# Optimization experiments

Hardware: AMD Instinct MI355X
Metric: run time of the kernel (lower is better)

Reference implementation:

```python
import jax, jax.numpy as jnp
import numpy as np

NEG_INF = -1e30  # mask value used by QANet's apply_mask


def setup_inputs() -> dict:
    key = jax.random.key(0)
    ks = jax.random.split(key, 6)
    B, C, Q, H = 64, 1024, 128, 512
    return {
        "x_context": jax.random.normal(ks[0], (B, C, H), dtype=jnp.float32),
        "x_query": jax.random.normal(ks[1], (B, Q, H), dtype=jnp.float32),
        "context_mask": jnp.ones((B, C), dtype=jnp.float32),
        "query_mask": jnp.ones((B, Q), dtype=jnp.float32),
        "W0": jax.random.normal(ks[2], (H,), dtype=jnp.float32) * 0.05,
        "W1": jax.random.normal(ks[3], (H,), dtype=jnp.float32) * 0.05,
        "W2": jax.random.normal(ks[4], (H,), dtype=jnp.float32) * 0.05,
        "bias": jnp.zeros((1,), dtype=jnp.float32),
    }


def reference(x_context, x_query, context_mask, query_mask, W0, W1, W2, bias):
    # Trilinear similarity S[b,c,q] = q.W0 + c.W1 + (q*W2).c + bias
    # (original computes [B,Q,C] then transposes; we build [B,C,Q] directly)
    sub0 = jnp.einsum('bqh,h->bq', x_query, W0)          # [B,Q]
    sub1 = jnp.einsum('bch,h->bc', x_context, W1)        # [B,C]
    sub2 = jnp.einsum('bch,bqh->bcq', x_context, x_query * W2)  # [B,C,Q]
    S = sub2 + sub1[:, :, None] + sub0[:, None, :] + bias  # [B,C,Q]

    mq = query_mask[:, None, :]    # [B,1,Q]
    mc = context_mask[:, :, None]  # [B,C,1]

    # context-to-query: softmax over query axis, masked by query_mask
    S_ = jax.nn.softmax(S + (1.0 - mq) * NEG_INF, axis=-1)  # [B,C,Q]
    c2q = jnp.einsum('bcq,bqh->bch', S_, x_query)           # [B,C,H]

    # query-to-context: softmax over context axis, masked by context_mask
    S_c = jax.nn.softmax(S + (1.0 - mc) * NEG_INF, axis=1)  # [B,C,Q]
    S_T = jnp.swapaxes(S_c, 1, 2)                            # [B,Q,C]
    # (S_ @ S_T) @ x_context, associated as S_ @ (S_T @ x_context)
    tmp = jnp.einsum('bqc,bch->bqh', S_T, x_context)        # [B,Q,H]
    q2c = jnp.einsum('bcq,bqh->bch', S_, tmp)               # [B,C,H]
    return c2q, q2c
```

## Files before the change

### kernel.cpp

```cpp
#include <hip/hip_runtime.h>

#define BB 64
#define CC 1024
#define QQ 128
#define HH 512

typedef short bf16x8 __attribute__((ext_vector_type(8)));
typedef float f32x4 __attribute__((ext_vector_type(4)));

#define GLD16(g, l)                                                            \
    __builtin_amdgcn_global_load_lds(                                          \
        (const __attribute__((address_space(1))) unsigned int*)(g),            \
        (__attribute__((address_space(3))) unsigned int*)(l), 16, 0, 0)

__device__ __forceinline__ unsigned short f2bf(float f) {
    unsigned u = __float_as_uint(f);
    u += 0x7FFF + ((u >> 16) & 1);
    return (unsigned short)(u >> 16);
}
__device__ __forceinline__ unsigned pk2(float lo, float hi) {
    return (unsigned)f2bf(lo) | ((unsigned)f2bf(hi) << 16);
}

__global__ __launch_bounds__(256) void k_sub0(const float* __restrict__ xq,
                                              const float* __restrict__ w0,
                                              float* __restrict__ sub0,
                                              float* __restrict__ colsum) {
    if (blockIdx.x < 32) colsum[blockIdx.x * 256 + threadIdx.x] = 0.0f;
    int wave = threadIdx.x >> 6;
    int lane = threadIdx.x & 63;
    int row  = blockIdx.x * 4 + wave;
    const float* p = xq + (size_t)row * HH + lane * 8;
    float4 a0 = *(const float4*)(p);
    float4 a1 = *(const float4*)(p + 4);
    float4 b0 = *(const float4*)(w0 + lane * 8);
    float4 b1 = *(const float4*)(w0 + lane * 8 + 4);
    float s = a0.x*b0.x + a0.y*b0.y + a0.z*b0.z + a0.w*b0.w
            + a1.x*b1.x + a1.y*b1.y + a1.z*b1.z + a1.w*b1.w;
    #pragma unroll
    for (int off = 32; off; off >>= 1) s += __shfl_xor(s, off);
    if (lane == 0) sub0[row] = s;
}

__global__ __launch_bounds__(256) void k_prep(const float* __restrict__ xq,
                                              const float* __restrict__ w2,
                                              const float* __restrict__ qmask,
                                              unsigned short* __restrict__ xqw2b,
                                              unsigned short* __restrict__ xqmT) {
    int b  = blockIdx.y;
    int ht = blockIdx.x * 128;
    int tid = threadIdx.x;
    __shared__ __align__(16) unsigned short sT[128][132];

    {
        int q  = tid >> 1;
        int hh = (tid & 1) * 64;
        float qm = qmask[b * QQ + q];
        const float* xp = xq + ((size_t)b * QQ + q) * HH + ht + hh;
        unsigned short* wr = xqw2b + ((size_t)b * QQ + q) * HH + ht + hh;
        #pragma unroll
        for (int i = 0; i < 16; i++) {
            float4 v = *(const float4*)(xp + i * 4);
            float4 w = *(const float4*)(w2 + ht + hh + i * 4);
            uint2 pw; pw.x = pk2(v.x * w.x, v.y * w.y);
                      pw.y = pk2(v.z * w.z, v.w * w.w);
            *(uint2*)(wr + i * 4) = pw;
            uint2 pm; pm.x = pk2(v.x * qm, v.y * qm);
                      pm.y = pk2(v.z * qm, v.w * qm);
            *(uint2*)(&sT[q][hh + i * 4]) = pm;
        }
    }
    __syncthreads();
    {
        int h  = tid >> 1;
        int qh = (tid & 1) * 64;
        unsigned short* orow = xqmT + ((size_t)b * HH + ht + h) * QQ + qh;
        #pragma unroll
        for (int i = 0; i < 8; i++) {
            uint4 o;
            o.x = (unsigned)sT[qh + i*8 + 0][h] | ((unsigned)sT[qh + i*8 + 1][h] << 16);
            o.y = (unsigned)sT[qh + i*8 + 2][h] | ((unsigned)sT[qh + i*8 + 3][h] << 16);
            o.z = (unsigned)sT[qh + i*8 + 4][h] | ((unsigned)sT[qh + i*8 + 5][h] << 16);
            o.w = (unsigned)sT[qh + i*8 + 6][h] | ((unsigned)sT[qh + i*8 + 7][h] << 16);
            *(uint4*)(orow + i * 8) = o;
        }
    }
}

__global__ __launch_bounds__(256) void k_scores(
    const float* __restrict__ xc, const unsigned short* __restrict__ xqw2b,
    const float* __restrict__ w1, const float* __restrict__ cmask,
    const float* __restrict__ qmask, const float* __restrict__ bias,
    const float* __restrict__ sub0, unsigned short* __restrict__ Ebf,
    float* __restrict__ rowsum, float* __restrict__ colsum) {
    int b  = blockIdx.y;
    int c0 = blockIdx.x * 128;
    int tid  = threadIdx.x;
    int lane = tid & 63, wave = tid >> 6;
    int quad = lane >> 4, lcol = lane & 15;
    int wrow = (wave >> 1) * 64, wcol = (wave & 1) * 64;

    __shared__ __align__(16) unsigned short sA[128][32];
    __shared__ __align__(16) unsigned short sB[128][32];
    __shared__ float sW1[512];
    __shared__ float sSub1[128];
    __shared__ float sS0[128], sQm[128], sCm[128];
    __shared__ float sRowP[2][128], sColP[2][128];

    sW1[tid] = w1[tid]; sW1[tid + 256] = w1[tid + 256];
    if (tid < 128) {
        sS0[tid] = sub0[b * QQ + tid] + bias[0];
        sQm[tid] = qmask[b * QQ + tid];
        sCm[tid] = cmask[b * CC + c0 + tid];
    }

    f32x4 acc[4][4];
    #pragma unroll
    for (int i = 0; i < 4; i++)
        #pragma unroll
        for (int j = 0; j < 4; j++) acc[i][j] = (f32x4)0.0f;
    float s1 = 0.0f;

    int arow = tid >> 1, akh = (tid & 1) * 16;

    for (int k0 = 0; k0 < HH; k0 += 32) {
        __syncthreads();
        {
            const float* gp = xc + ((size_t)(b * CC + c0 + arow)) * HH + k0 + akh;
            float4 v0 = *(const float4*)(gp);
            float4 v1 = *(const float4*)(gp + 4);
            float4 v2 = *(const float4*)(gp + 8);
            float4 v3 = *(const float4*)(gp + 12);
            const float* wp = sW1 + k0 + akh;
            s1 += v0.x*wp[0] + v0.y*wp[1] + v0.z*wp[2] + v0.w*wp[3]
                + v1.x*wp[4] + v1.y*wp[5] + v1.z*wp[6] + v1.w*wp[7]
                + v2.x*wp[8] + v2.y*wp[9] + v2.z*wp[10] + v2.w*wp[11]
                + v3.x*wp[12] + v3.y*wp[13] + v3.z*wp[14] + v3.w*wp[15];
            uint4 p0, p1;
            p0.x = pk2(v0.x, v0.y); p0.y = pk2(v0.z, v0.w);
            p0.z = pk2(v1.x, v1.y); p0.w = pk2(v1.z, v1.w);
            p1.x = pk2(v2.x, v2.y); p1.y = pk2(v2.z, v2.w);
            p1.z = pk2(v3.x, v3.y); p1.w = pk2(v3.z, v3.w);
            *(uint4*)&sA[arow][akh]     = p0;
            *(uint4*)&sA[arow][akh + 8] = p1;
        }
        #pragma unroll
        for (int j = 0; j < 2; j++) {
            int chunk = wave * 2 + j;
            int row = chunk * 16 + (lane >> 2);
            GLD16(xqw2b + ((size_t)b * QQ + row) * HH + k0 + (lane & 3) * 8,
                  (unsigned short*)sB + chunk * 512);
        }
        __syncthreads();
        bf16x8 af[4];
        #pragma unroll
        for (int mi = 0; mi < 4; mi++)
            af[mi] = *(const bf16x8*)&sA[wrow + mi * 16 + lcol][quad * 8];
        #pragma unroll
        for (int ni = 0; ni < 4; ni++) {
            bf16x8 bfr = *(const bf16x8*)&sB[wcol + ni * 16 + lcol][quad * 8];
            #pragma unroll
            for (int mi = 0; mi < 4; mi++)
                acc[mi][ni] = __builtin_amdgcn_mfma_f32_16x16x32_bf16(
                    af[mi], bfr, acc[mi][ni], 0, 0, 0);
        }
    }

    s1 += __shfl_xor(s1, 1);
    if ((tid & 1) == 0) sSub1[arow] = s1;
    __syncthreads();

    float rsp[4][4];
    float csp[4] = {0.f, 0.f, 0.f, 0.f};
    #pragma unroll
    for (int mi = 0; mi < 4; mi++)
        #pragma unroll
        for (int r = 0; r < 4; r++) rsp[mi][r] = 0.f;

    #pragma unroll
    for (int mi = 0; mi < 4; mi++) {
        #pragma unroll
        for (int ni = 0; ni < 4; ni++) {
            int col = wcol + ni * 16 + lcol;
            float qm = sQm[col], s0 = sS0[col];
            #pragma unroll
            for (int r = 0; r < 4; r++) {
                int row = wrow + mi * 16 + quad * 4 + r;
                float e = __expf(acc[mi][ni][r] + sSub1[row] + s0);
                acc[mi][ni][r] = e;
                rsp[mi][r] += e * qm;
                csp[ni] += e * sCm[row];
            }
        }
    }
    #pragma unroll
    for (int mi = 0; mi < 4; mi++)
        #pragma unroll
        for (int r = 0; r < 4; r++) {
            float v = rsp[mi][r];
            v += __shfl_xor(v, 1); v += __shfl_xor(v, 2);
            v += __shfl_xor(v, 4); v += __shfl_xor(v, 8);
            if (lcol == 0) sRowP[wave & 1][wrow + mi * 16 + quad * 4 + r] = v;
        }
    #pragma unroll
    for (int ni = 0; ni < 4; ni++) {
        float v = csp[ni];
        v += __shfl_xor(v, 16); v += __shfl_xor(v, 32);
        if (quad == 0) sColP[wave >> 1][wcol + ni * 16 + lcol] = v;
    }
    #pragma unroll
    for (int mi = 0; mi < 4; mi++)
        #pragma unroll
        for (int ni = 0; ni < 4; ni++) {
            int col = wcol + ni * 16 + lcol;
            #pragma unroll
            for (int r = 0; r < 4; r++) {
                int row = wrow + mi * 16 + quad * 4 + r;
                Ebf[((size_t)(b * CC + c0 + row)) * QQ + col] = f2bf(acc[mi][ni][r]);
            }
        }
    __syncthreads();
    if (tid < 128) {
        rowsum[(size_t)b * CC + c0 + tid] = sRowP[0][tid] + sRowP[1][tid];
        atomicAdd(&colsum[b * QQ + tid], sColP[0][tid] + sColP[1][tid]);
    }
}

__global__ __launch_bounds__(256) void k_tmp(
    const unsigned short* __restrict__ Ebf, const float* __restrict__ xc,
    const float* __restrict__ cmask, const float* __restrict__ qmask,
    const float* __restrict__ colsum, unsigned short* __restrict__ tmpT) {
    int b  = blockIdx.y;
    int h0 = blockIdx.x * 64;
    int tid  = threadIdx.x;
    int lane = tid & 63, wave = tid >> 6;
    int quad = lane >> 4, lcol = lane & 15;
    int wrow = (wave >> 1) * 64;
    int wcol = (wave & 1) * 32;

    __shared__ __align__(16) unsigned int sAu[128 * 16];
    __shared__ __align__(16) unsigned int sBu[64 * 16];
    __shared__ float sInv[128];
    if (tid < 128) sInv[tid] = qmask[b * QQ + tid] / colsum[b * QQ + tid];

    f32x4 acc[4][2];
    #pragma unroll
    for (int i = 0; i < 4; i++) { acc[i][0] = (f32x4)0.f; acc[i][1] = (f32x4)0.f; }

    int tp = tid >> 4;
    int tq = tid & 15;

    for (int c0 = 0; c0 < CC; c0 += 32) {
        __syncthreads();
        {
            const unsigned short* ep = Ebf + ((size_t)b * CC + c0 + 2 * tp) * QQ + tq * 8;
            union { uint4 v; unsigned short s[8]; } r0, r1;
            r0.v = *(const uint4*)ep;
            r1.v = *(const uint4*)(ep + QQ);
            #pragma unroll
            for (int j = 0; j < 8; j++) {
                int q = tq * 8 + j;
                unsigned pk = (unsigned)r0.s[j] | ((unsigned)r1.s[j] << 16);
                sAu[q * 16 + (((tp >> 2) ^ (q >> 3 & 3)) << 2) + (tp & 3)] = pk;
            }
        }
        {
            const float* xp = xc + ((size_t)b * CC + c0 + 2 * tp) * HH + h0 + tq * 4;
            float cm0 = cmask[b * CC + c0 + 2 * tp];
            float cm1 = cmask[b * CC + c0 + 2 * tp + 1];
            float4 f0 = *(const float4*)xp;
            float4 f1 = *(const float4*)(xp + HH);
            float a0[4] = {f0.x, f0.y, f0.z, f0.w};
            float a1[4] = {f1.x, f1.y, f1.z, f1.w};
            #pragma unroll
            for (int j = 0; j < 4; j++) {
                int h = tq * 4 + j;
                unsigned pk = pk2(a0[j] * cm0, a1[j] * cm1);
                sBu[h * 16 + (((tp >> 2) ^ (h >> 3 & 3)) << 2) + (tp & 3)] = pk;
            }
        }
        __syncthreads();
        bf16x8 af[4];
        #pragma unroll
        for (int mi = 0; mi < 4; mi++) {
            int m = wrow + mi * 16 + lcol;
            af[mi] = *(const bf16x8*)(sAu + m * 16 + ((quad ^ (m >> 3 & 3)) << 2));
        }
        #pragma unroll
        for (int ni = 0; ni < 2; ni++) {
            int n = wcol + ni * 16 + lcol;
            bf16x8 bfr = *(const bf16x8*)(sBu + n * 16 + ((quad ^ (n >> 3 & 3)) << 2));
            #pragma unroll
            for (int mi = 0; mi < 4; mi++)
                acc[mi][ni] = __builtin_amdgcn_mfma_f32_16x16x32_bf16(
                    af[mi], bfr, acc[mi][ni], 0, 0, 0);
        }
    }
    #pragma unroll
    for (int mi = 0; mi < 4; mi++) {
        int qb = wrow + mi * 16 + quad * 4;
        #pragma unroll
        for (int ni = 0; ni < 2; ni++) {
            int h = wcol + ni * 16 + lcol;
            uint2 o;
            o.x = pk2(acc[mi][ni][0] * sInv[qb + 0], acc[mi][ni][1] * sInv[qb + 1]);
            o.y = pk2(acc[mi][ni][2] * sInv[qb + 2], acc[mi][ni][3] * sInv[qb + 3]);
            *(uint2*)(tmpT + ((size_t)b * HH + h0 + h) * QQ + qb) = o;
        }
    }
}

__global__ __launch_bounds__(256) void k_out(
    const unsigned short* __restrict__ Ebf, const unsigned short* __restrict__ xqmT,
    const unsigned short* __restrict__ tmpT, const float* __restrict__ rowsum,
    float* __restrict__ c2q, float* __restrict__ q2c) {
    int b  = blockIdx.z;
    int c0 = blockIdx.y * 128;
    int h0 = blockIdx.x * 128;
    int tid  = threadIdx.x;
    int lane = tid & 63, wave = tid >> 6;
    int quad = lane >> 4, lcol = lane & 15;
    int wrow = (wave >> 1) * 64, wcol = (wave & 1) * 64;

    __shared__ __align__(16) unsigned short sA[128][32];
    __shared__ __align__(16) unsigned short sB1[128][32];
    __shared__ __align__(16) unsigned short sB2[128][32];
    __shared__ float sInvR[128];
    if (tid < 128) sInvR[tid] = 1.0f / rowsum[(size_t)b * CC + c0 + tid];

    f32x4 acc1[4][4], acc2[4][4];
    #pragma unroll
    for (int i = 0; i < 4; i++)
        #pragma unroll
        for (int j = 0; j < 4; j++) { acc1[i][j] = (f32x4)0.f; acc2[i][j] = (f32x4)0.f; }

    for (int k0 = 0; k0 < QQ; k0 += 32) {
        __syncthreads();
        #pragma unroll
        for (int j = 0; j < 2; j++) {
            int chunk = wave * 2 + j;
            int row = chunk * 16 + (lane >> 2);
            int kb  = (lane & 3) * 8;
            GLD16(Ebf  + ((size_t)b * CC + c0 + row) * QQ + k0 + kb,
                  (unsigned short*)sA + chunk * 512);
            GLD16(xqmT + ((size_t)b * HH + h0 + row) * QQ + k0 + kb,
                  (unsigned short*)sB1 + chunk * 512);
            GLD16(tmpT + ((size_t)b * HH + h0 + row) * QQ + k0 + kb,
                  (unsigned short*)sB2 + chunk * 512);
        }
        __syncthreads();
        bf16x8 af[4];
        #pragma unroll
        for (int mi = 0; mi < 4; mi++)
            af[mi] = *(const bf16x8*)&sA[wrow + mi * 16 + lcol][quad * 8];
        #pragma unroll
        for (int ni = 0; ni < 4; ni++) {
            bf16x8 b1 = *(const bf16x8*)&sB1[wcol + ni * 16 + lcol][quad * 8];
            bf16x8 b2 = *(const bf16x8*)&sB2[wcol + ni * 16 + lcol][quad * 8];
            #pragma unroll
            for (int mi = 0; mi < 4; mi++) {
                acc1[mi][ni] = __builtin_amdgcn_mfma_f32_16x16x32_bf16(
                    af[mi], b1, acc1[mi][ni], 0, 0, 0);
                acc2[mi][ni] = __builtin_amdgcn_mfma_f32_16x16x32_bf16(
                    af[mi], b2, acc2[mi][ni], 0, 0, 0);
            }
        }
    }
    #pragma unroll
    for (int mi = 0; mi < 4; mi++) {
        int rb = wrow + mi * 16 + quad * 4;
        float ir0 = sInvR[rb], ir1 = sInvR[rb + 1], ir2 = sInvR[rb + 2], ir3 = sInvR[rb + 3];
        #pragma unroll
        for (int ni = 0; ni < 4; ni++) {
            int col = h0 + wcol + ni * 16 + lcol;
            size_t o0 = ((size_t)b * CC + c0 + rb) * HH + col;
            c2q[o0]          = acc1[mi][ni][0] * ir0;
            c2q[o0 + HH]     = acc1[mi][ni][1] * ir1;
            c2q[o0 + 2*HH]   = acc1[mi][ni][2] * ir2;
            c2q[o0 + 3*HH]   = acc1[mi][ni][3] * ir3;
            q2c[o0]          = acc2[mi][ni][0] * ir0;
            q2c[o0 + HH]     = acc2[mi][ni][1] * ir1;
            q2c[o0 + 2*HH]   = acc2[mi][ni][2] * ir2;
            q2c[o0 + 3*HH]   = acc2[mi][ni][3] * ir3;
        }
    }
}

extern "C" void kernel_launch(void* const* d_in, const int* in_sizes, int n_in,
                              void* d_out, int out_size, void* d_ws, size_t ws_size,
                              hipStream_t stream) {
    const float* xc    = (const float*)d_in[0];
    const float* xq    = (const float*)d_in[1];
    const float* cmask = (const float*)d_in[2];
    const float* qmask = (const float*)d_in[3];
    const float* w0    = (const float*)d_in[4];
    const float* w1    = (const float*)d_in[5];
    const float* w2    = (const float*)d_in[6];
    const float* bias  = (const float*)d_in[7];

    float* out = (float*)d_out;
    float* c2q = out;
    float* q2c = out + (size_t)BB * CC * HH;

    unsigned short* Ebf   = (unsigned short*)d_ws;
    unsigned short* xqw2b = Ebf   + (size_t)BB * CC * QQ;
    unsigned short* xqmT  = xqw2b + (size_t)BB * QQ * HH;
    unsigned short* tmpT  = xqmT  + (size_t)BB * QQ * HH;
    float* rowsum = (float*)(tmpT + (size_t)BB * QQ * HH);
    float* colsum = rowsum + (size_t)BB * CC;
    float* sub0   = colsum + (size_t)BB * QQ;

    k_sub0  <<<dim3(BB * QQ / 4),      256, 0, stream>>>(xq, w0, sub0, colsum);
    k_prep  <<<dim3(HH / 128, BB),     256, 0, stream>>>(xq, w2, qmask, xqw2b, xqmT);
    k_scores<<<dim3(CC / 128, BB),     256, 0, stream>>>(xc, xqw2b, w1, cmask, qmask,
                                                         bias, sub0, Ebf, rowsum, colsum);
    k_tmp   <<<dim3(HH / 64, BB),      256, 0, stream>>>(Ebf, xc, cmask, qmask,
                                                         colsum, tmpT);
    k_out   <<<dim3(HH / 128, CC / 128, BB), 256, 0, stream>>>(Ebf, xqmT, tmpT,
                                                               rowsum, c2q, q2c);
}
```

Measured before the change: 477.1 us.

## Precompute bf16 context and transposed layouts in a prep kernel for async LDS loads

Adds a k_prep_c kernel that converts x_context to bf16, computes sub1, and writes a cmask-scaled transposed copy. k_scores now also writes a transposed copy of the exp-score matrix. k_scores and k_tmp can then stream operands with direct global-to-LDS loads, and k_tmp moves to 128x128 tiles. This removes in-loop fp32 conversion and the LDS transpose/swizzle work. In exchange it adds an extra pass over x_context plus extra workspace writes and reads for xcb, xcmT and EbfT.

Result: slower. 545.7 us (+14.4%).

```diff
diff --git a/kernel.cpp b/kernel.cpp
--- a/kernel.cpp
+++ b/kernel.cpp
@@ -42,11 +42,11 @@
     if (lane == 0) sub0[row] = s;
 }
 
-__global__ __launch_bounds__(256) void k_prep(const float* __restrict__ xq,
-                                              const float* __restrict__ w2,
-                                              const float* __restrict__ qmask,
-                                              unsigned short* __restrict__ xqw2b,
-                                              unsigned short* __restrict__ xqmT) {
+__global__ __launch_bounds__(256) void k_prep_q(const float* __restrict__ xq,
+                                                const float* __restrict__ w2,
+                                                const float* __restrict__ qmask,
+                                                unsigned short* __restrict__ xqw2b,
+                                                unsigned short* __restrict__ xqmT) {
     int b  = blockIdx.y;
     int ht = blockIdx.x * 128;
     int tid = threadIdx.x;
@@ -87,12 +87,74 @@
     }
 }
 
+__global__ __launch_bounds__(256) void k_prep_c(const float* __restrict__ xc,
+                                                const float* __restrict__ w1,
+                                                const float* __restrict__ cmask,
+                                                unsigned short* __restrict__ xcb,
+                                                unsigned short* __restrict__ xcmT,
+                                                float* __restrict__ sub1) {
+    int b  = blockIdx.y;
+    int c0 = blockIdx.x * 128;
+    int tid = threadIdx.x;
+    int lane = tid & 63, w = tid >> 6;
+    __shared__ __align__(16) unsigned short sX[32 * 520];
+    __shared__ float sW1[512];
+    sW1[tid] = w1[tid]; sW1[tid + 256] = w1[tid + 256];
+    __syncthreads();
+
+    for (int g = 0; g < 4; g++) {
+        #pragma unroll
+        for (int i = 0; i < 8; i++) {
+            int rl = i * 4 + w;
+            int c  = c0 + g * 32 + rl;
+            const float* xp = xc + ((size_t)b * CC + c) * HH + lane * 8;
+            float4 v0 = *(const float4*)xp;
+            float4 v1 = *(const float4*)(xp + 4);
+            float cm = cmask[b * CC + c];
+            const float* wp = sW1 + lane * 8;
+            float d = v0.x*wp[0] + v0.y*wp[1] + v0.z*wp[2] + v0.w*wp[3]
+                    + v1.x*wp[4] + v1.y*wp[5] + v1.z*wp[6] + v1.w*wp[7];
+            #pragma unroll
+            for (int off = 32; off; off >>= 1) d += __shfl_xor(d, off);
+            if (lane == 0) sub1[(size_t)b * CC + c] = d;
+            uint4 p;
+            p.x = pk2(v0.x, v0.y); p.y = pk2(v0.z, v0.w);
+            p.z = pk2(v1.x, v1.y); p.w = pk2(v1.z, v1.w);
+            *(uint4*)(xcb + ((size_t)b * CC + c) * HH + lane * 8) = p;
+            uint4 m;
+            m.x = pk2(v0.x * cm, v0.y * cm); m.y = pk2(v0.z * cm, v0.w * cm);
+            m.z = pk2(v1.x * cm, v1.y * cm); m.w = pk2(v1.z * cm, v1.w * cm);
+            *(uint4*)(sX + rl * 520 + lane * 8) = m;
+        }
+        __syncthreads();
+        {
+            unsigned wlo[16], whi[16];
+            #pragma unroll
+            for (int j = 0; j < 16; j++) {
+                unsigned u0 = *(const unsigned*)(sX + (2*j)     * 520 + 2 * tid);
+                unsigned u1 = *(const unsigned*)(sX + (2*j + 1) * 520 + 2 * tid);
+                wlo[j] = (u0 & 0xFFFFu) | (u1 << 16);
+                whi[j] = (u0 >> 16)     | (u1 & 0xFFFF0000u);
+            }
+            unsigned short* o0 = xcmT + ((size_t)b * HH + 2 * tid) * CC + c0 + g * 32;
+            unsigned short* o1 = o0 + CC;
+            #pragma unroll
+            for (int j = 0; j < 4; j++) {
+                *(uint4*)(o0 + j * 8) = *(uint4*)(wlo + j * 4);
+                *(uint4*)(o1 + j * 8) = *(uint4*)(whi + j * 4);
+            }
+        }
+        __syncthreads();
+    }
+}
+
 __global__ __launch_bounds__(256) void k_scores(
-    const float* __restrict__ xc, const unsigned short* __restrict__ xqw2b,
-    const float* __restrict__ w1, const float* __restrict__ cmask,
-    const float* __restrict__ qmask, const float* __restrict__ bias,
-    const float* __restrict__ sub0, unsigned short* __restrict__ Ebf,
-    float* __restrict__ rowsum, float* __restrict__ colsum) {
+    const unsigned short* __restrict__ xcb, const unsigned short* __restrict__ xqw2b,
+    const float* __restrict__ cmask, const float* __restrict__ qmask,
+    const float* __restrict__ bias, const float* __restrict__ sub0,
+    const float* __restrict__ sub1, unsigned short* __restrict__ Ebf,
+    unsigned short* __restrict__ EbfT, float* __restrict__ rowsum,
+    float* __restrict__ colsum) {
     int b  = blockIdx.y;
     int c0 = blockIdx.x * 128;
     int tid  = threadIdx.x;
@@ -100,15 +162,13 @@
     int quad = lane >> 4, lcol = lane & 15;
     int wrow = (wave >> 1) * 64, wcol = (wave & 1) * 64;
 
-    __shared__ __align__(16) unsigned short sA[128][32];
-    __shared__ __align__(16) unsigned short sB[128][32];
-    __shared__ float sW1[512];
-    __shared__ float sSub1[128];
-    __shared__ float sS0[128], sQm[128], sCm[128];
+    __shared__ __align__(16) unsigned short sA[128 * 32];
+    __shared__ __align__(16) unsigned short sB[128 * 32];
+    __shared__ float sS1[128], sS0[128], sQm[128], sCm[128];
     __shared__ float sRowP[2][128], sColP[2][128];
 
-    sW1[tid] = w1[tid]; sW1[tid + 256] = w1[tid + 256];
     if (tid < 128) {
+        sS1[tid] = sub1[(size_t)b * CC + c0 + tid];
         sS0[tid] = sub0[b * QQ + tid] + bias[0];
         sQm[tid] = qmask[b * QQ + tid];
         sCm[tid] = cmask[b * CC + c0 + tid];
@@ -119,46 +179,27 @@
     for (int i = 0; i < 4; i++)
         #pragma unroll
         for (int j = 0; j < 4; j++) acc[i][j] = (f32x4)0.0f;
-    float s1 = 0.0f;
-
-    int arow = tid >> 1, akh = (tid & 1) * 16;
 
     for (int k0 = 0; k0 < HH; k0 += 32) {
         __syncthreads();
-        {
-            const float* gp = xc + ((size_t)(b * CC + c0 + arow)) * HH + k0 + akh;
-            float4 v0 = *(const float4*)(gp);
-            float4 v1 = *(const float4*)(gp + 4);
-            float4 v2 = *(const float4*)(gp + 8);
-            float4 v3 = *(const float4*)(gp + 12);
-            const float* wp = sW1 + k0 + akh;
-            s1 += v0.x*wp[0] + v0.y*wp[1] + v0.z*wp[2] + v0.w*wp[3]
-                + v1.x*wp[4] + v1.y*wp[5] + v1.z*wp[6] + v1.w*wp[7]
-                + v2.x*wp[8] + v2.y*wp[9] + v2.z*wp[10] + v2.w*wp[11]
-                + v3.x*wp[12] + v3.y*wp[13] + v3.z*wp[14] + v3.w*wp[15];
-            uint4 p0, p1;
-            p0.x = pk2(v0.x, v0.y); p0.y = pk2(v0.z, v0.w);
-            p0.z = pk2(v1.x, v1.y); p0.w = pk2(v1.z, v1.w);
-            p1.x = pk2(v2.x, v2.y); p1.y = pk2(v2.z, v2.w);
-            p1.z = pk2(v3.x, v3.y); p1.w = pk2(v3.z, v3.w);
-            *(uint4*)&sA[arow][akh]     = p0;
-            *(uint4*)&sA[arow][akh + 8] = p1;
-        }
         #pragma unroll
         for (int j = 0; j < 2; j++) {
             int chunk = wave * 2 + j;
             int row = chunk * 16 + (lane >> 2);
-            GLD16(xqw2b + ((size_t)b * QQ + row) * HH + k0 + (lane & 3) * 8,
-                  (unsigned short*)sB + chunk * 512);
+            int kb  = (lane & 3) * 8;
+            GLD16(xcb   + ((size_t)(b * CC + c0 + row)) * HH + k0 + kb,
+                  sA + chunk * 512);
+            GLD16(xqw2b + ((size_t)(b * QQ + row)) * HH + k0 + kb,
+                  sB + chunk * 512);
         }
         __syncthreads();
         bf16x8 af[4];
         #pragma unroll
         for (int mi = 0; mi < 4; mi++)
-            af[mi] = *(const bf16x8*)&sA[wrow + mi * 16 + lcol][quad * 8];
-        #pragma unroll
-        for (int ni = 0; ni < 4; ni++) {
-            bf16x8 bfr = *(const bf16x8*)&sB[wcol + ni * 16 + lcol][quad * 8];
+            af[mi] = *(const bf16x8*)(sA + (wrow + mi * 16 + lcol) * 32 + quad * 8);
+        #pragma unroll
+        for (int ni = 0; ni < 4; ni++) {
+            bf16x8 bfr = *(const bf16x8*)(sB + (wcol + ni * 16 + lcol) * 32 + quad * 8);
             #pragma unroll
             for (int mi = 0; mi < 4; mi++)
                 acc[mi][ni] = __builtin_amdgcn_mfma_f32_16x16x32_bf16(
@@ -166,10 +207,6 @@
         }
     }
 
-    s1 += __shfl_xor(s1, 1);
-    if ((tid & 1) == 0) sSub1[arow] = s1;
-    __syncthreads();
-
     float rsp[4][4];
     float csp[4] = {0.f, 0.f, 0.f, 0.f};
     #pragma unroll
@@ -179,18 +216,25 @@
 
     #pragma unroll
     for (int mi = 0; mi < 4; mi++) {
+        int rb = wrow + mi * 16 + quad * 4;
         #pragma unroll
         for (int ni = 0; ni < 4; ni++) {
             int col = wcol + ni * 16 + lcol;
             float qm = sQm[col], s0 = sS0[col];
+            float ev[4];
             #pragma unroll
             for (int r = 0; r < 4; r++) {
-                int row = wrow + mi * 16 + quad * 4 + r;
-                float e = __expf(acc[mi][ni][r] + sSub1[row] + s0);
-                acc[mi][ni][r] = e;
+                int row = rb + r;
+                float e = __expf(acc[mi][ni][r] + sS1[row] + s0);
+                ev[r] = e;
                 rsp[mi][r] += e * qm;
                 csp[ni] += e * sCm[row];
+                Ebf[((size_t)(b * CC + c0 + row)) * QQ + col] = f2bf(e);
             }
+            uint2 o;
+            o.x = pk2(ev[0], ev[1]);
+            o.y = pk2(ev[2], ev[3]);
+            *(uint2*)(EbfT + ((size_t)(b * QQ + col)) * CC + c0 + rb) = o;
         }
     }
     #pragma unroll
@@ -208,17 +252,6 @@
         v += __shfl_xor(v, 16); v += __shfl_xor(v, 32);
         if (quad == 0) sColP[wave >> 1][wcol + ni * 16 + lcol] = v;
     }
-    #pragma unroll
-    for (int mi = 0; mi < 4; mi++)
-        #pragma unroll
-        for (int ni = 0; ni < 4; ni++) {
-            int col = wcol + ni * 16 + lcol;
-            #pragma unroll
-            for (int r = 0; r < 4; r++) {
-                int row = wrow + mi * 16 + quad * 4 + r;
-                Ebf[((size_t)(b * CC + c0 + row)) * QQ + col] = f2bf(acc[mi][ni][r]);
-            }
-        }
     __syncthreads();
     if (tid < 128) {
         rowsum[(size_t)b * CC + c0 + tid] = sRowP[0][tid] + sRowP[1][tid];
@@ -227,69 +260,47 @@
 }
 
 __global__ __launch_bounds__(256) void k_tmp(
-    const unsigned short* __restrict__ Ebf, const float* __restrict__ xc,
-    const float* __restrict__ cmask, const float* __restrict__ qmask,
-    const float* __restrict__ colsum, unsigned short* __restrict__ tmpT) {
+    const unsigned short* __restrict__ xcmT, const unsigned short* __restrict__ EbfT,
+    const float* __restrict__ qmask, const float* __restrict__ colsum,
+    unsigned short* __restrict__ tmpT) {
     int b  = blockIdx.y;
-    int h0 = blockIdx.x * 64;
+    int h0 = blockIdx.x * 128;
     int tid  = threadIdx.x;
     int lane = tid & 63, wave = tid >> 6;
     int quad = lane >> 4, lcol = lane & 15;
-    int wrow = (wave >> 1) * 64;
-    int wcol = (wave & 1) * 32;
-
-    __shared__ __align__(16) unsigned int sAu[128 * 16];
-    __shared__ __align__(16) unsigned int sBu[64 * 16];
+    int wrow = (wave >> 1) * 64, wcol = (wave & 1) * 64;
+
+    __shared__ __align__(16) unsigned short sA[128 * 32];
+    __shared__ __align__(16) unsigned short sB[128 * 32];
     __shared__ float sInv[128];
     if (tid < 128) sInv[tid] = qmask[b * QQ + tid] / colsum[b * QQ + tid];
 
-    f32x4 acc[4][2];
-    #pragma unroll
-    for (int i = 0; i < 4; i++) { acc[i][0] = (f32x4)0.f; acc[i][1] = (f32x4)0.f; }
-
-    int tp = tid >> 4;
-    int tq = tid & 15;
-
-    for (int c0 = 0; c0 < CC; c0 += 32) {
-        __syncthreads();
-        {
-            const unsigned short* ep = Ebf + ((size_t)b * CC + c0 + 2 * tp) * QQ + tq * 8;
-            union { uint4 v; unsigned short s[8]; } r0, r1;
-            r0.v = *(const uint4*)ep;
-            r1.v = *(const uint4*)(ep + QQ);
-            #pragma unroll
-            for (int j = 0; j < 8; j++) {
-                int q = tq * 8 + j;
-                unsigned pk = (unsigned)r0.s[j] | ((unsigned)r1.s[j] << 16);
-                sAu[q * 16 + (((tp >> 2) ^ (q >> 3 & 3)) << 2) + (tp & 3)] = pk;
-            }
-        }
-        {
-            const float* xp = xc + ((size_t)b * CC + c0 + 2 * tp) * HH + h0 + tq * 4;
-            float cm0 = cmask[b * CC + c0 + 2 * tp];
-            float cm1 = cmask[b * CC + c0 + 2 * tp + 1];
-            float4 f0 = *(const float4*)xp;
-            float4 f1 = *(const float4*)(xp + HH);
-            float a0[4] = {f0.x, f0.y, f0.z, f0.w};
-            float a1[4] = {f1.x, f1.y, f1.z, f1.w};
-            #pragma unroll
-            for (int j = 0; j < 4; j++) {
-                int h = tq * 4 + j;
-                unsigned pk = pk2(a0[j] * cm0, a1[j] * cm1);
-                sBu[h * 16 + (((tp >> 2) ^ (h >> 3 & 3)) << 2) + (tp & 3)] = pk;
-            }
+    f32x4 acc[4][4];
+    #pragma unroll
+    for (int i = 0; i < 4; i++)
+        #pragma unroll
+        for (int j = 0; j < 4; j++) acc[i][j] = (f32x4)0.0f;
+
+    for (int c0k = 0; c0k < CC; c0k += 32) {
+        __syncthreads();
+        #pragma unroll
+        for (int j = 0; j < 2; j++) {
+            int chunk = wave * 2 + j;
+            int row = chunk * 16 + (lane >> 2);
+            int kb  = (lane & 3) * 8;
+            GLD16(xcmT + ((size_t)(b * HH + h0 + row)) * CC + c0k + kb,
+                  sA + chunk * 512);
+            GLD16(EbfT + ((size_t)(b * QQ + row)) * CC + c0k + kb,
+                  sB + chunk * 512);
         }
         __syncthreads();
         bf16x8 af[4];
         #pragma unroll
-        for (int mi = 0; mi < 4; mi++) {
-            int m = wrow + mi * 16 + lcol;
-            af[mi] = *(const bf16x8*)(sAu + m * 16 + ((quad ^ (m >> 3 & 3)) << 2));
-        }
-        #pragma unroll
-        for (int ni = 0; ni < 2; ni++) {
-            int n = wcol + ni * 16 + lcol;
-            bf16x8 bfr = *(const bf16x8*)(sBu + n * 16 + ((quad ^ (n >> 3 & 3)) << 2));
+        for (int mi = 0; mi < 4; mi++)
+            af[mi] = *(const bf16x8*)(sA + (wrow + mi * 16 + lcol) * 32 + quad * 8);
+        #pragma unroll
+        for (int ni = 0; ni < 4; ni++) {
+            bf16x8 bfr = *(const bf16x8*)(sB + (wcol + ni * 16 + lcol) * 32 + quad * 8);
             #pragma unroll
             for (int mi = 0; mi < 4; mi++)
                 acc[mi][ni] = __builtin_amdgcn_mfma_f32_16x16x32_bf16(
@@ -298,14 +309,15 @@
     }
     #pragma unroll
     for (int mi = 0; mi < 4; mi++) {
-        int qb = wrow + mi * 16 + quad * 4;
-        #pragma unroll
-        for (int ni = 0; ni < 2; ni++) {
-            int h = wcol + ni * 16 + lcol;
-            uint2 o;
-            o.x = pk2(acc[mi][ni][0] * sInv[qb + 0], acc[mi][ni][1] * sInv[qb + 1]);
-            o.y = pk2(acc[mi][ni][2] * sInv[qb + 2], acc[mi][ni][3] * sInv[qb + 3]);
-            *(uint2*)(tmpT + ((size_t)b * HH + h0 + h) * QQ + qb) = o;
+        int hb = wrow + mi * 16 + quad * 4;
+        #pragma unroll
+        for (int ni = 0; ni < 4; ni++) {
+            int q = wcol + ni * 16 + lcol;
+            float iv = sInv[q];
+            #pragma unroll
+            for (int r = 0; r < 4; r++)
+                tmpT[((size_t)(b * HH + h0 + hb + r)) * QQ + q] =
+                    f2bf(acc[mi][ni][r] * iv);
         }
     }
 }
@@ -322,9 +334,9 @@
     int quad = lane >> 4, lcol = lane & 15;
     int wrow = (wave >> 1) * 64, wcol = (wave & 1) * 64;
 
-    __shared__ __align__(16) unsigned short sA[128][32];
-    __shared__ __align__(16) unsigned short sB1[128][32];
-    __shared__ __align__(16) unsigned short sB2[128][32];
+    __shared__ __align__(16) unsigned short sA[128 * 32];
+    __shared__ __align__(16) unsigned short sB1[128 * 32];
+    __shared__ __align__(16) unsigned short sB2[128 * 32];
     __shared__ float sInvR[128];
     if (tid < 128) sInvR[tid] = 1.0f / rowsum[(size_t)b * CC + c0 + tid];
 
@@ -341,22 +353,22 @@
             int chunk = wave * 2 + j;
             int row = chunk * 16 + (lane >> 2);
             int kb  = (lane & 3) * 8;
-            GLD16(Ebf  + ((size_t)b * CC + c0 + row) * QQ + k0 + kb,
-                  (unsigned short*)sA + chunk * 512);
-            GLD16(xqmT + ((size_t)b * HH + h0 + row) * QQ + k0 + kb,
-                  (unsigned short*)sB1 + chunk * 512);
-            GLD16(tmpT + ((size_t)b * HH + h0 + row) * QQ + k0 + kb,
-                  (unsigned short*)sB2 + chunk * 512);
+            GLD16(Ebf  + ((size_t)(b * CC + c0 + row)) * QQ + k0 + kb,
+                  sA + chunk * 512);
+            GLD16(xqmT + ((size_t)(b * HH + h0 + row)) * QQ + k0 + kb,
+                  sB1 + chunk * 512);
+            GLD16(tmpT + ((size_t)(b * HH + h0 + row)) * QQ + k0 + kb,
+                  sB2 + chunk * 512);
         }
         __syncthreads();
         bf16x8 af[4];
         #pragma unroll
         for (int mi = 0; mi < 4; mi++)
-            af[mi] = *(const bf16x8*)&sA[wrow + mi * 16 + lcol][quad * 8];
-        #pragma unroll
-        for (int ni = 0; ni < 4; ni++) {
-            bf16x8 b1 = *(const bf16x8*)&sB1[wcol + ni * 16 + lcol][quad * 8];
-            bf16x8 b2 = *(const bf16x8*)&sB2[wcol + ni * 16 + lcol][quad * 8];
+            af[mi] = *(const bf16x8*)(sA + (wrow + mi * 16 + lcol) * 32 + quad * 8);
+        #pragma unroll
+        for (int ni = 0; ni < 4; ni++) {
+            bf16x8 b1 = *(const bf16x8*)(sB1 + (wcol + ni * 16 + lcol) * 32 + quad * 8);
+            bf16x8 b2 = *(const bf16x8*)(sB2 + (wcol + ni * 16 + lcol) * 32 + quad * 8);
             #pragma unroll
             for (int mi = 0; mi < 4; mi++) {
                 acc1[mi][ni] = __builtin_amdgcn_mfma_f32_16x16x32_bf16(
@@ -373,15 +385,15 @@
         #pragma unroll
         for (int ni = 0; ni < 4; ni++) {
             int col = h0 + wcol + ni * 16 + lcol;
-            size_t o0 = ((size_t)b * CC + c0 + rb) * HH + col;
-            c2q[o0]          = acc1[mi][ni][0] * ir0;
-            c2q[o0 + HH]     = acc1[mi][ni][1] * ir1;
-            c2q[o0 + 2*HH]   = acc1[mi][ni][2] * ir2;
-            c2q[o0 + 3*HH]   = acc1[mi][ni][3] * ir3;
-            q2c[o0]          = acc2[mi][ni][0] * ir0;
-            q2c[o0 + HH]     = acc2[mi][ni][1] * ir1;
-            q2c[o0 + 2*HH]   = acc2[mi][ni][2] * ir2;
-            q2c[o0 + 3*HH]   = acc2[mi][ni][3] * ir3;
+            size_t o0 = ((size_t)(b * CC + c0 + rb)) * HH + col;
+            c2q[o0]        = acc1[mi][ni][0] * ir0;
+            c2q[o0 + HH]   = acc1[mi][ni][1] * ir1;
+            c2q[o0 + 2*HH] = acc1[mi][ni][2] * ir2;
+            c2q[o0 + 3*HH] = acc1[mi][ni][3] * ir3;
+            q2c[o0]        = acc2[mi][ni][0] * ir0;
+            q2c[o0 + HH]   = acc2[mi][ni][1] * ir1;
+            q2c[o0 + 2*HH] = acc2[mi][ni][2] * ir2;
+            q2c[o0 + 3*HH] = acc2[mi][ni][3] * ir3;
         }
     }
 }
@@ -403,19 +415,25 @@
     float* q2c = out + (size_t)BB * CC * HH;
 
     unsigned short* Ebf   = (unsigned short*)d_ws;
-    unsigned short* xqw2b = Ebf   + (size_t)BB * CC * QQ;
+    unsigned short* EbfT  = Ebf   + (size_t)BB * CC * QQ;
+    unsigned short* xqw2b = EbfT  + (size_t)BB * QQ * CC;
     unsigned short* xqmT  = xqw2b + (size_t)BB * QQ * HH;
     unsigned short* tmpT  = xqmT  + (size_t)BB * QQ * HH;
-    float* rowsum = (float*)(tmpT + (size_t)BB * QQ * HH);
+    unsigned short* xcb   = tmpT  + (size_t)BB * HH * QQ;
+    unsigned short* xcmT  = xcb   + (size_t)BB * CC * HH;
+    float* rowsum = (float*)(xcmT + (size_t)BB * HH * CC);
     float* colsum = rowsum + (size_t)BB * CC;
     float* sub0   = colsum + (size_t)BB * QQ;
-
-    k_sub0  <<<dim3(BB * QQ / 4),      256, 0, stream>>>(xq, w0, sub0, colsum);
-    k_prep  <<<dim3(HH / 128, BB),     256, 0, stream>>>(xq, w2, qmask, xqw2b, xqmT);
-    k_scores<<<dim3(CC / 128, BB),     256, 0, stream>>>(xc, xqw2b, w1, cmask, qmask,
-                                                         bias, sub0, Ebf, rowsum, colsum);
-    k_tmp   <<<dim3(HH / 64, BB),      256, 0, stream>>>(Ebf, xc, cmask, qmask,
-                                                         colsum, tmpT);
+    float* sub1   = sub0   + (size_t)BB * QQ;
+
+    k_sub0  <<<dim3(BB * QQ / 4),        256, 0, stream>>>(xq, w0, sub0, colsum);
+    k_prep_q<<<dim3(HH / 128, BB),       256, 0, stream>>>(xq, w2, qmask, xqw2b, xqmT);
+    k_prep_c<<<dim3(CC / 128, BB),       256, 0, stream>>>(xc, w1, cmask, xcb, xcmT, sub1);
+    k_scores<<<dim3(CC / 128, BB),       256, 0, stream>>>(xcb, xqw2b, cmask, qmask,
+                                                           bias, sub0, sub1,
+                                                           Ebf, EbfT, rowsum, colsum);
+    k_tmp   <<<dim3(HH / 128, BB),       256, 0, stream>>>(xcmT, EbfT, qmask,
+                                                           colsum, tmpT);
     k_out   <<<dim3(HH / 128, CC / 128, BB), 256, 0, stream>>>(Ebf, xqmT, tmpT,
                                                                rowsum, c2q, q2c);
 }
```
